# Optimization experiments

Hardware: AMD Instinct MI355X
Metric: run time of the kernel (lower is better)

The kernel has to match this reference:

```python
import jax, jax.numpy as jnp
import numpy as np

LN_EPS = 1e-5
WINDOWS = (5, 10, 20)


def _rolling_vol_mean(returns, w):
    # returns: [B, L]; rolling unbiased std (torch.std, ddof=1) over window w,
    # then mean over all window positions -> [B, 1]
    B = returns.shape[0]
    z = jnp.zeros((B, 1), returns.dtype)
    c1 = jnp.concatenate([z, jnp.cumsum(returns, axis=1)], axis=1)
    c2 = jnp.concatenate([z, jnp.cumsum(returns * returns, axis=1)], axis=1)
    s1 = c1[:, w:] - c1[:, :-w]          # window sums      [B, L-w+1]
    s2 = c2[:, w:] - c2[:, :-w]          # window sq sums   [B, L-w+1]
    var = (s2 - s1 * s1 / w) / (w - 1)
    std = jnp.sqrt(jnp.maximum(var, 0.0))
    return jnp.mean(std, axis=1, keepdims=True)


def _layernorm(x, g, b):
    mu = jnp.mean(x, axis=-1, keepdims=True)
    v = jnp.mean((x - mu) ** 2, axis=-1, keepdims=True)
    return (x - mu) / jnp.sqrt(v + LN_EPS) * g + b


def setup_inputs() -> dict:
    key = jax.random.key(0)
    ks = jax.random.split(key, 8)
    B, S, F = 4096, 4096, 1
    input_dim, hidden = 64, 256
    h2 = hidden // 2
    price_series = jax.random.uniform(ks[0], (B, S, F), jnp.float32) + 0.5
    sd = 0.02
    return {
        "price_series": price_series,
        "W1": jax.random.normal(ks[1], (input_dim, h2), jnp.float32) * sd,
        "b1": jnp.zeros((h2,), jnp.float32),
        "g1": jnp.ones((h2,), jnp.float32),
        "be1": jnp.zeros((h2,), jnp.float32),
        "W2": jax.random.normal(ks[2], (h2, h2), jnp.float32) * sd,
        "b2": jnp.zeros((h2,), jnp.float32),
        "g2": jnp.ones((h2,), jnp.float32),
        "be2": jnp.zeros((h2,), jnp.float32),
        "Wc1": jax.random.normal(ks[3], (hidden, 64), jnp.float32) * sd,
        "bc1": jnp.zeros((64,), jnp.float32),
        "Wc2": jax.random.normal(ks[4], (64, 4), jnp.float32) * sd,
        "bc2": jnp.zeros((4,), jnp.float32),
    }


def reference(price_series, W1, b1, g1, be1, W2, b2, g2, be2, Wc1, bc1, Wc2, bc2):
    input_dim = W1.shape[0]
    # features == 1 path: log returns
    safe_prices = jnp.clip(price_series, 1e-8, None)
    log_prices = jnp.log(safe_prices)
    returns = (log_prices[:, 1:, 0] - log_prices[:, :-1, 0])  # [B, S-1]

    vol_feats = [_rolling_vol_mean(returns, w) for w in WINDOWS]
    vol = jnp.concatenate(vol_feats, axis=1)                  # [B, 3]
    B = vol.shape[0]
    pad = jnp.zeros((B, input_dim - vol.shape[1]), vol.dtype)
    vol = jnp.concatenate([vol, pad], axis=1)                 # [B, input_dim]

    h = _layernorm(jax.nn.relu(vol @ W1 + b1), g1, be1)       # [B, h2]
    h2f = _layernorm(jax.nn.relu(h @ W2 + b2), g2, be2)       # [B, h2]
    combined = jnp.concatenate([h, h2f], axis=1)              # [B, hidden]
    logits = jax.nn.relu(combined @ Wc1 + bc1) @ Wc2 + bc2    # dropout = identity at eval
    regime = jax.nn.softmax(logits, axis=1)
    return combined, regime
```

## Files before the change

kernel.cpp:

```cpp
#include <hip/hip_runtime.h>
#include <math.h>

constexpr int S   = 4096;
constexpr int L   = S - 1;
constexpr int H2  = 128;
constexpr int HID = 256;
constexpr int NPOS = 16;
constexpr int WMAX = 20;
constexpr int RMAX = NPOS + WMAX - 1;
constexpr float LN_EPS = 1e-5f;

__device__ __forceinline__ float fast_sqrt(float x) { return __builtin_amdgcn_sqrtf(x); }
__device__ __forceinline__ float fast_rsqrt(float x) { return __builtin_amdgcn_rsqf(x); }

__device__ __forceinline__ float2 block_sum2(float a, float b, int tid, float* red8) {
    #pragma unroll
    for (int off = 32; off; off >>= 1) {
        a += __shfl_down(a, off);
        b += __shfl_down(b, off);
    }
    if ((tid & 63) == 0) { red8[(tid >> 6) * 2] = a; red8[(tid >> 6) * 2 + 1] = b; }
    __syncthreads();
    float2 r = make_float2(red8[0] + red8[2] + red8[4] + red8[6],
                           red8[1] + red8[3] + red8[5] + red8[7]);
    __syncthreads();
    return r;
}

template<int W>
__device__ __forceinline__ float window_acc(const float (&rr)[RMAX], int t0) {
    float s1 = 0.f, s2 = 0.f;
    #pragma unroll
    for (int j = 0; j < W; ++j) { s1 += rr[j]; s2 = fmaf(rr[j], rr[j], s2); }
    float acc = 0.f;
    constexpr float invw   = 1.f / (float)W;
    constexpr float invwm1 = 1.f / (float)(W - 1);
    const int n = L - W + 1;
    #pragma unroll
    for (int i = 0; i < NPOS; ++i) {
        if (t0 + i < n) {
            float var = (s2 - s1 * s1 * invw) * invwm1;
            acc += fast_sqrt(fmaxf(var, 0.f));
        }
        if (i < NPOS - 1) {
            float xin = rr[i + W], xout = rr[i];
            s1 += xin - xout;
            s2 += fmaf(xin, xin, -(xout * xout));
        }
    }
    return acc;
}

__global__ __launch_bounds__(256)
void vol_fused(const float* __restrict__ prices,
               const float* __restrict__ W1,  const float* __restrict__ b1,
               const float* __restrict__ g1,  const float* __restrict__ be1,
               const float* __restrict__ W2,  const float* __restrict__ b2,
               const float* __restrict__ g2,  const float* __restrict__ be2,
               const float* __restrict__ Wc1, const float* __restrict__ bc1,
               const float* __restrict__ Wc2, const float* __restrict__ bc2,
               float* __restrict__ out_combined, float* __restrict__ out_regime)
{
    __shared__ __align__(16) float lp[S + 40];
    __shared__ __align__(16) float part[1024];
    __shared__ float red8[8];
    __shared__ float redv[16];
    __shared__ float comb[HID];
    __shared__ float vols[4];

    const int tid = threadIdx.x;
    const int b   = blockIdx.x;

    const float4* prow = reinterpret_cast<const float4*>(prices + (size_t)b * S);
    #pragma unroll
    for (int i = 0; i < S / (4 * 256); ++i) {
        int idx = tid + i * 256;
        float4 v = prow[idx];
        lp[idx * 4 + 0] = __logf(fmaxf(v.x, 1e-8f));
        lp[idx * 4 + 1] = __logf(fmaxf(v.y, 1e-8f));
        lp[idx * 4 + 2] = __logf(fmaxf(v.z, 1e-8f));
        lp[idx * 4 + 3] = __logf(fmaxf(v.w, 1e-8f));
    }
    if (tid < 40) lp[S + tid] = 0.f;
    __syncthreads();

    const int t0 = tid * NPOS;
    float lpv[RMAX + 1];
    #pragma unroll
    for (int i = 0; i < (RMAX + 1) / 4; ++i) {
        float4 v = *reinterpret_cast<const float4*>(&lp[t0 + 4 * i]);
        lpv[4 * i + 0] = v.x; lpv[4 * i + 1] = v.y;
        lpv[4 * i + 2] = v.z; lpv[4 * i + 3] = v.w;
    }
    float rr[RMAX];
    #pragma unroll
    for (int i = 0; i < RMAX; ++i) rr[i] = lpv[i + 1] - lpv[i];

    float sum5  = window_acc<5>(rr, t0);
    float sum10 = window_acc<10>(rr, t0);
    float sum20 = window_acc<20>(rr, t0);

    #pragma unroll
    for (int off = 32; off; off >>= 1) {
        sum5  += __shfl_down(sum5,  off);
        sum10 += __shfl_down(sum10, off);
        sum20 += __shfl_down(sum20, off);
    }
    if ((tid & 63) == 0) {
        int w = tid >> 6;
        redv[w * 3 + 0] = sum5; redv[w * 3 + 1] = sum10; redv[w * 3 + 2] = sum20;
    }
    __syncthreads();
    if (tid < 3) {
        constexpr float sc[3] = { 1.f / (L - 5 + 1), 1.f / (L - 10 + 1), 1.f / (L - 20 + 1) };
        vols[tid] = (redv[tid] + redv[3 + tid] + redv[6 + tid] + redv[9 + tid]) * sc[tid];
    }
    __syncthreads();

    const float v0 = vols[0], v1 = vols[1], v2 = vols[2];

    float x = 0.f;
    if (tid < H2) {
        x = b1[tid];
        x = fmaf(v0, W1[0 * H2 + tid], x);
        x = fmaf(v1, W1[1 * H2 + tid], x);
        x = fmaf(v2, W1[2 * H2 + tid], x);
        x = fmaxf(x, 0.f);
    }
    float2 s = block_sum2((tid < H2) ? x : 0.f, (tid < H2) ? x * x : 0.f, tid, red8);
    {
        float mu  = s.x * (1.f / H2);
        float var = s.y * (1.f / H2) - mu * mu;
        if (tid < H2)
            comb[tid] = (x - mu) * fast_rsqrt(fmaxf(var, 0.f) + LN_EPS) * g1[tid] + be1[tid];
    }
    __syncthreads();

    {
        const int q = tid & 31, seg = tid >> 3 >> 2;
        const float* w2base = W2 + (size_t)(seg * 16) * H2 + q * 4;
        float ax = 0.f, ay = 0.f, az = 0.f, aw = 0.f;
        #pragma unroll
        for (int k = 0; k < 16; ++k) {
            float a = comb[seg * 16 + k];
            float4 w = *reinterpret_cast<const float4*>(w2base + (size_t)k * H2);
            ax = fmaf(a, w.x, ax); ay = fmaf(a, w.y, ay);
            az = fmaf(a, w.z, az); aw = fmaf(a, w.w, aw);
        }
        float4* p4 = reinterpret_cast<float4*>(part);
        p4[tid] = make_float4(ax, ay, az, aw);
    }
    __syncthreads();
    float x2 = 0.f;
    if (tid < H2) {
        float ssum = 0.f;
        #pragma unroll
        for (int sg = 0; sg < 8; ++sg) ssum += part[sg * 128 + tid];
        x2 = fmaxf(ssum + b2[tid], 0.f);
    }
    s = block_sum2((tid < H2) ? x2 : 0.f, (tid < H2) ? x2 * x2 : 0.f, tid, red8);
    {
        float mu  = s.x * (1.f / H2);
        float var = s.y * (1.f / H2) - mu * mu;
        if (tid < H2)
            comb[H2 + tid] = (x2 - mu) * fast_rsqrt(fmaxf(var, 0.f) + LN_EPS) * g2[tid] + be2[tid];
    }
    __syncthreads();

    out_combined[(size_t)b * HID + tid] = comb[tid];

    {
        const int q = tid & 15, seg = tid >> 4;
        const float* wcbase = Wc1 + (size_t)(seg * 16) * 64 + q * 4;
        float ax = 0.f, ay = 0.f, az = 0.f, aw = 0.f;
        #pragma unroll
        for (int k = 0; k < 16; ++k) {
            float a = comb[seg * 16 + k];
            float4 w = *reinterpret_cast<const float4*>(wcbase + (size_t)k * 64);
            ax = fmaf(a, w.x, ax); ay = fmaf(a, w.y, ay);
            az = fmaf(a, w.z, az); aw = fmaf(a, w.w, aw);
        }
        float4* p4 = reinterpret_cast<float4*>(part);
        p4[tid] = make_float4(ax, ay, az, aw);
    }
    __syncthreads();

    if (tid < 64) {
        float ssum = 0.f;
        #pragma unroll
        for (int sg = 0; sg < 16; ++sg) ssum += part[sg * 64 + tid];
        float c1 = fmaxf(ssum + bc1[tid], 0.f);

        float4 wrow = reinterpret_cast<const float4*>(Wc2)[tid];
        float lx = c1 * wrow.x, ly = c1 * wrow.y, lz = c1 * wrow.z, lw = c1 * wrow.w;
        #pragma unroll
        for (int off = 32; off; off >>= 1) {
            lx += __shfl_down(lx, off);
            ly += __shfl_down(ly, off);
            lz += __shfl_down(lz, off);
            lw += __shfl_down(lw, off);
        }
        if (tid == 0) {
            float4 bb = *reinterpret_cast<const float4*>(bc2);
            float l0 = lx + bb.x, l1 = ly + bb.y, l2 = lz + bb.z, l3 = lw + bb.w;
            float m  = fmaxf(fmaxf(l0, l1), fmaxf(l2, l3));
            float e0 = __expf(l0 - m), e1 = __expf(l1 - m);
            float e2 = __expf(l2 - m), e3 = __expf(l3 - m);
            float inv = 1.f / (e0 + e1 + e2 + e3);
            reinterpret_cast<float4*>(out_regime)[b] =
                make_float4(e0 * inv, e1 * inv, e2 * inv, e3 * inv);
        }
    }
}

extern "C" void kernel_launch(void* const* d_in, const int* in_sizes, int n_in,
                              void* d_out, int out_size, void* d_ws, size_t ws_size,
                              hipStream_t stream) {
    const float* prices = (const float*)d_in[0];
    const float* W1  = (const float*)d_in[1];
    const float* b1  = (const float*)d_in[2];
    const float* g1  = (const float*)d_in[3];
    const float* be1 = (const float*)d_in[4];
    const float* W2  = (const float*)d_in[5];
    const float* b2  = (const float*)d_in[6];
    const float* g2  = (const float*)d_in[7];
    const float* be2 = (const float*)d_in[8];
    const float* Wc1 = (const float*)d_in[9];
    const float* bc1 = (const float*)d_in[10];
    const float* Wc2 = (const float*)d_in[11];
    const float* bc2 = (const float*)d_in[12];

    const int B = in_sizes[0] / S;
    float* out_combined = (float*)d_out;
    float* out_regime   = (float*)d_out + (size_t)B * HID;

    vol_fused<<<B, 256, 0, stream>>>(prices, W1, b1, g1, be1, W2, b2, g2, be2,
                                     Wc1, bc1, Wc2, bc2, out_combined, out_regime);
}
```

Measured before the change: 43.86 us.

## Process two rows per block with register prefix sums, dropping shared log buffer

Each block now handles two batch rows. Each thread loads its own overlapping slice of prices straight from global memory into registers and takes logs there, so the shared log-price staging buffer and its barrier are gone. Rolling window std is computed from per-thread prefix sums instead of three sliding accumulators, and the MLP stages are restructured so all 256 threads work on both rows at once, amortizing weight loads. The cost is redundant global loads and log computations for the overlapping window halo, plus higher register pressure under the new occupancy hint.

```diff
diff --git a/kernel.cpp b/kernel.cpp
--- a/kernel.cpp
+++ b/kernel.cpp
@@ -1,198 +1,200 @@
 #include <hip/hip_runtime.h>
 #include <math.h>
 
-constexpr int S   = 4096;
-constexpr int L   = S - 1;
-constexpr int H2  = 128;
-constexpr int HID = 256;
+constexpr int S    = 4096;
+constexpr int L    = S - 1;
+constexpr int H2   = 128;
+constexpr int HID  = 256;
 constexpr int NPOS = 16;
-constexpr int WMAX = 20;
-constexpr int RMAX = NPOS + WMAX - 1;
+constexpr int ROWS = 2;
 constexpr float LN_EPS = 1e-5f;
 
-__device__ __forceinline__ float fast_sqrt(float x) { return __builtin_amdgcn_sqrtf(x); }
+constexpr int N5  = L - 5 + 1;
+constexpr int N10 = L - 10 + 1;
+constexpr int N20 = L - 20 + 1;
+
+__device__ __forceinline__ float fast_sqrt(float x)  { return __builtin_amdgcn_sqrtf(x); }
 __device__ __forceinline__ float fast_rsqrt(float x) { return __builtin_amdgcn_rsqf(x); }
 
-__device__ __forceinline__ float2 block_sum2(float a, float b, int tid, float* red8) {
-    #pragma unroll
-    for (int off = 32; off; off >>= 1) {
-        a += __shfl_down(a, off);
-        b += __shfl_down(b, off);
-    }
-    if ((tid & 63) == 0) { red8[(tid >> 6) * 2] = a; red8[(tid >> 6) * 2 + 1] = b; }
-    __syncthreads();
-    float2 r = make_float2(red8[0] + red8[2] + red8[4] + red8[6],
-                           red8[1] + red8[3] + red8[5] + red8[7]);
-    __syncthreads();
-    return r;
+template<int W>
+__device__ __forceinline__ float wstd(const float (&c1)[36], const float (&c2)[36], int i) {
+    constexpr float aw = 1.f / (float)(W - 1);
+    constexpr float bw = 1.f / ((float)W * (float)(W - 1));
+    float s1 = c1[i + W] - c1[i];
+    float s2 = c2[i + W] - c2[i];
+    float t  = fmaf(-(s1 * bw), s1, s2 * aw);
+    return fast_sqrt(fmaxf(t, 0.f));
 }
 
-template<int W>
-__device__ __forceinline__ float window_acc(const float (&rr)[RMAX], int t0) {
-    float s1 = 0.f, s2 = 0.f;
-    #pragma unroll
-    for (int j = 0; j < W; ++j) { s1 += rr[j]; s2 = fmaf(rr[j], rr[j], s2); }
-    float acc = 0.f;
-    constexpr float invw   = 1.f / (float)W;
-    constexpr float invwm1 = 1.f / (float)(W - 1);
-    const int n = L - W + 1;
-    #pragma unroll
-    for (int i = 0; i < NPOS; ++i) {
-        if (t0 + i < n) {
-            float var = (s2 - s1 * s1 * invw) * invwm1;
-            acc += fast_sqrt(fmaxf(var, 0.f));
-        }
-        if (i < NPOS - 1) {
-            float xin = rr[i + W], xout = rr[i];
-            s1 += xin - xout;
-            s2 += fmaf(xin, xin, -(xout * xout));
-        }
-    }
-    return acc;
-}
-
-__global__ __launch_bounds__(256)
-void vol_fused(const float* __restrict__ prices,
-               const float* __restrict__ W1,  const float* __restrict__ b1,
-               const float* __restrict__ g1,  const float* __restrict__ be1,
-               const float* __restrict__ W2,  const float* __restrict__ b2,
-               const float* __restrict__ g2,  const float* __restrict__ be2,
-               const float* __restrict__ Wc1, const float* __restrict__ bc1,
-               const float* __restrict__ Wc2, const float* __restrict__ bc2,
-               float* __restrict__ out_combined, float* __restrict__ out_regime)
+__global__ __launch_bounds__(256, 4)
+void vol_fused2(const float* __restrict__ prices,
+                const float* __restrict__ W1,  const float* __restrict__ b1,
+                const float* __restrict__ g1,  const float* __restrict__ be1,
+                const float* __restrict__ W2,  const float* __restrict__ b2,
+                const float* __restrict__ g2,  const float* __restrict__ be2,
+                const float* __restrict__ Wc1, const float* __restrict__ bc1,
+                const float* __restrict__ Wc2, const float* __restrict__ bc2,
+                float* __restrict__ out_combined, float* __restrict__ out_regime)
 {
-    __shared__ __align__(16) float lp[S + 40];
-    __shared__ __align__(16) float part[1024];
-    __shared__ float red8[8];
-    __shared__ float redv[16];
-    __shared__ float comb[HID];
-    __shared__ float vols[4];
+    __shared__ __align__(16) float fbuf[ROWS * HID];
+    __shared__ __align__(16) float partb[1024];
+    __shared__ float redw[ROWS][4][3];
+    __shared__ float vols_sh[ROWS][4];
+    __shared__ float c1s_unused[4];
 
     const int tid = threadIdx.x;
-    const int b   = blockIdx.x;
-
-    const float4* prow = reinterpret_cast<const float4*>(prices + (size_t)b * S);
-    #pragma unroll
-    for (int i = 0; i < S / (4 * 256); ++i) {
-        int idx = tid + i * 256;
-        float4 v = prow[idx];
-        lp[idx * 4 + 0] = __logf(fmaxf(v.x, 1e-8f));
-        lp[idx * 4 + 1] = __logf(fmaxf(v.y, 1e-8f));
-        lp[idx * 4 + 2] = __logf(fmaxf(v.z, 1e-8f));
-        lp[idx * 4 + 3] = __logf(fmaxf(v.w, 1e-8f));
-    }
-    if (tid < 40) lp[S + tid] = 0.f;
-    __syncthreads();
-
-    const int t0 = tid * NPOS;
-    float lpv[RMAX + 1];
-    #pragma unroll
-    for (int i = 0; i < (RMAX + 1) / 4; ++i) {
-        float4 v = *reinterpret_cast<const float4*>(&lp[t0 + 4 * i]);
-        lpv[4 * i + 0] = v.x; lpv[4 * i + 1] = v.y;
-        lpv[4 * i + 2] = v.z; lpv[4 * i + 3] = v.w;
-    }
-    float rr[RMAX];
-    #pragma unroll
-    for (int i = 0; i < RMAX; ++i) rr[i] = lpv[i + 1] - lpv[i];
-
-    float sum5  = window_acc<5>(rr, t0);
-    float sum10 = window_acc<10>(rr, t0);
-    float sum20 = window_acc<20>(rr, t0);
-
-    #pragma unroll
-    for (int off = 32; off; off >>= 1) {
-        sum5  += __shfl_down(sum5,  off);
-        sum10 += __shfl_down(sum10, off);
-        sum20 += __shfl_down(sum20, off);
-    }
-    if ((tid & 63) == 0) {
-        int w = tid >> 6;
-        redv[w * 3 + 0] = sum5; redv[w * 3 + 1] = sum10; redv[w * 3 + 2] = sum20;
-    }
-    __syncthreads();
-    if (tid < 3) {
-        constexpr float sc[3] = { 1.f / (L - 5 + 1), 1.f / (L - 10 + 1), 1.f / (L - 20 + 1) };
-        vols[tid] = (redv[tid] + redv[3 + tid] + redv[6 + tid] + redv[9 + tid]) * sc[tid];
-    }
-    __syncthreads();
-
-    const float v0 = vols[0], v1 = vols[1], v2 = vols[2];
-
-    float x = 0.f;
-    if (tid < H2) {
-        x = b1[tid];
-        x = fmaf(v0, W1[0 * H2 + tid], x);
-        x = fmaf(v1, W1[1 * H2 + tid], x);
-        x = fmaf(v2, W1[2 * H2 + tid], x);
-        x = fmaxf(x, 0.f);
-    }
-    float2 s = block_sum2((tid < H2) ? x : 0.f, (tid < H2) ? x * x : 0.f, tid, red8);
-    {
-        float mu  = s.x * (1.f / H2);
-        float var = s.y * (1.f / H2) - mu * mu;
-        if (tid < H2)
-            comb[tid] = (x - mu) * fast_rsqrt(fmaxf(var, 0.f) + LN_EPS) * g1[tid] + be1[tid];
-    }
-    __syncthreads();
-
-    {
-        const int q = tid & 31, seg = tid >> 3 >> 2;
-        const float* w2base = W2 + (size_t)(seg * 16) * H2 + q * 4;
+    const int w   = tid >> 6;
+    const int r0  = blockIdx.x * ROWS;
+
+    #pragma unroll 1
+    for (int r = 0; r < ROWS; ++r) {
+        const float4* p4 = reinterpret_cast<const float4*>(prices + (size_t)(r0 + r) * S);
+        float v[36];
+        #pragma unroll
+        for (int j = 0; j < 9; ++j) {
+            int sl = tid * 4 + j;
+            sl = sl < 1024 ? sl : 1023;
+            float4 f = p4[sl];
+            v[4 * j + 0] = f.x; v[4 * j + 1] = f.y;
+            v[4 * j + 2] = f.z; v[4 * j + 3] = f.w;
+        }
+        #pragma unroll
+        for (int i = 0; i < 36; ++i) v[i] = __logf(fmaxf(v[i], 1e-8f));
+
+        float c1[36], c2[36];
+        c1[0] = 0.f; c2[0] = 0.f;
+        #pragma unroll
+        for (int k = 1; k < 36; ++k) {
+            float d = v[k] - v[k - 1];
+            c1[k] = c1[k - 1] + d;
+            c2[k] = fmaf(d, d, c2[k - 1]);
+        }
+
+        const int t0 = tid * NPOS;
+        float sum5 = 0.f, sum10 = 0.f, sum20 = 0.f;
+        if (t0 + NPOS <= N20) {
+            #pragma unroll
+            for (int i = 0; i < NPOS; ++i) {
+                sum5  += wstd<5>(c1, c2, i);
+                sum10 += wstd<10>(c1, c2, i);
+                sum20 += wstd<20>(c1, c2, i);
+            }
+        } else {
+            #pragma unroll
+            for (int i = 0; i < NPOS; ++i) {
+                float s5 = wstd<5>(c1, c2, i), s10 = wstd<10>(c1, c2, i), s20 = wstd<20>(c1, c2, i);
+                if (t0 + i < N5)  sum5  += s5;
+                if (t0 + i < N10) sum10 += s10;
+                if (t0 + i < N20) sum20 += s20;
+            }
+        }
+        #pragma unroll
+        for (int off = 32; off; off >>= 1) {
+            sum5  += __shfl_down(sum5,  off);
+            sum10 += __shfl_down(sum10, off);
+            sum20 += __shfl_down(sum20, off);
+        }
+        if ((tid & 63) == 0) {
+            redw[r][w][0] = sum5; redw[r][w][1] = sum10; redw[r][w][2] = sum20;
+        }
+    }
+    __syncthreads();
+    if (tid < ROWS * 3) {
+        int r = tid / 3, k = tid % 3;
+        constexpr float sc[3] = { 1.f / N5, 1.f / N10, 1.f / N20 };
+        vols_sh[r][k] = (redw[r][0][k] + redw[r][1][k] + redw[r][2][k] + redw[r][3][k]) * sc[k];
+    }
+    __syncthreads();
+
+    const int c  = tid & 127;
+    const int rw = tid >> 7;
+    float x = fmaxf(fmaf(vols_sh[rw][2], W1[2 * H2 + c],
+                    fmaf(vols_sh[rw][1], W1[H2 + c],
+                    fmaf(vols_sh[rw][0], W1[c], b1[c]))), 0.f);
+    {
+        float s = x, sq = x * x;
+        #pragma unroll
+        for (int off = 32; off; off >>= 1) { s += __shfl_down(s, off); sq += __shfl_down(sq, off); }
+        if ((tid & 63) == 0) { redw[0][w][0] = s; redw[0][w][1] = sq; }
+    }
+    __syncthreads();
+    {
+        float ss = redw[0][rw * 2][0] + redw[0][rw * 2 + 1][0];
+        float sq = redw[0][rw * 2][1] + redw[0][rw * 2 + 1][1];
+        float mu = ss * (1.f / H2);
+        float var = sq * (1.f / H2) - mu * mu;
+        float rs = fast_rsqrt(fmaxf(var, 0.f) + LN_EPS);
+        fbuf[rw * HID + c] = (x - mu) * rs * g1[c] + be1[c];
+    }
+    __syncthreads();
+
+    {
+        const int q = tid & 31, r2 = (tid >> 5) & 1, kq = tid >> 6;
+        const float* wb = W2 + (size_t)(kq * 32) * H2 + q * 4;
+        const float* ab = &fbuf[r2 * HID + kq * 32];
         float ax = 0.f, ay = 0.f, az = 0.f, aw = 0.f;
-        #pragma unroll
-        for (int k = 0; k < 16; ++k) {
-            float a = comb[seg * 16 + k];
-            float4 w = *reinterpret_cast<const float4*>(w2base + (size_t)k * H2);
-            ax = fmaf(a, w.x, ax); ay = fmaf(a, w.y, ay);
-            az = fmaf(a, w.z, az); aw = fmaf(a, w.w, aw);
-        }
-        float4* p4 = reinterpret_cast<float4*>(part);
-        p4[tid] = make_float4(ax, ay, az, aw);
-    }
-    __syncthreads();
-    float x2 = 0.f;
-    if (tid < H2) {
-        float ssum = 0.f;
-        #pragma unroll
-        for (int sg = 0; sg < 8; ++sg) ssum += part[sg * 128 + tid];
-        x2 = fmaxf(ssum + b2[tid], 0.f);
-    }
-    s = block_sum2((tid < H2) ? x2 : 0.f, (tid < H2) ? x2 * x2 : 0.f, tid, red8);
-    {
-        float mu  = s.x * (1.f / H2);
-        float var = s.y * (1.f / H2) - mu * mu;
-        if (tid < H2)
-            comb[H2 + tid] = (x2 - mu) * fast_rsqrt(fmaxf(var, 0.f) + LN_EPS) * g2[tid] + be2[tid];
-    }
-    __syncthreads();
-
-    out_combined[(size_t)b * HID + tid] = comb[tid];
-
-    {
-        const int q = tid & 15, seg = tid >> 4;
-        const float* wcbase = Wc1 + (size_t)(seg * 16) * 64 + q * 4;
+        #pragma unroll 8
+        for (int k = 0; k < 32; ++k) {
+            float a = ab[k];
+            float4 ww = *reinterpret_cast<const float4*>(wb + (size_t)k * H2);
+            ax = fmaf(a, ww.x, ax); ay = fmaf(a, ww.y, ay);
+            az = fmaf(a, ww.z, az); aw = fmaf(a, ww.w, aw);
+        }
+        reinterpret_cast<float4*>(partb)[tid] = make_float4(ax, ay, az, aw);
+    }
+    __syncthreads();
+    float x2;
+    {
+        const int qq = c >> 2, ci = c & 3;
+        float ss = partb[(0 * 64 + rw * 32 + qq) * 4 + ci] +
+                   partb[(1 * 64 + rw * 32 + qq) * 4 + ci] +
+                   partb[(2 * 64 + rw * 32 + qq) * 4 + ci] +
+                   partb[(3 * 64 + rw * 32 + qq) * 4 + ci];
+        x2 = fmaxf(ss + b2[c], 0.f);
+    }
+    {
+        float s = x2, sq = x2 * x2;
+        #pragma unroll
+        for (int off = 32; off; off >>= 1) { s += __shfl_down(s, off); sq += __shfl_down(sq, off); }
+        if ((tid & 63) == 0) { redw[0][w][0] = s; redw[0][w][1] = sq; }
+    }
+    __syncthreads();
+    {
+        float ss = redw[0][rw * 2][0] + redw[0][rw * 2 + 1][0];
+        float sq = redw[0][rw * 2][1] + redw[0][rw * 2 + 1][1];
+        float mu = ss * (1.f / H2);
+        float var = sq * (1.f / H2) - mu * mu;
+        float rs = fast_rsqrt(fmaxf(var, 0.f) + LN_EPS);
+        fbuf[rw * HID + H2 + c] = (x2 - mu) * rs * g2[c] + be2[c];
+    }
+    __syncthreads();
+
+    {
+        const int cq = tid & 15, r2 = (tid >> 4) & 1, kq = tid >> 5;
+        const float* wb = Wc1 + (size_t)(kq * 32) * 64 + cq * 4;
+        const float* ab = &fbuf[r2 * HID + kq * 32];
         float ax = 0.f, ay = 0.f, az = 0.f, aw = 0.f;
-        #pragma unroll
-        for (int k = 0; k < 16; ++k) {
-            float a = comb[seg * 16 + k];
-            float4 w = *reinterpret_cast<const float4*>(wcbase + (size_t)k * 64);
-            ax = fmaf(a, w.x, ax); ay = fmaf(a, w.y, ay);
-            az = fmaf(a, w.z, az); aw = fmaf(a, w.w, aw);
-        }
-        float4* p4 = reinterpret_cast<float4*>(part);
-        p4[tid] = make_float4(ax, ay, az, aw);
-    }
-    __syncthreads();
-
-    if (tid < 64) {
-        float ssum = 0.f;
-        #pragma unroll
-        for (int sg = 0; sg < 16; ++sg) ssum += part[sg * 64 + tid];
-        float c1 = fmaxf(ssum + bc1[tid], 0.f);
-
-        float4 wrow = reinterpret_cast<const float4*>(Wc2)[tid];
-        float lx = c1 * wrow.x, ly = c1 * wrow.y, lz = c1 * wrow.z, lw = c1 * wrow.w;
+        #pragma unroll 8
+        for (int k = 0; k < 32; ++k) {
+            float a = ab[k];
+            float4 ww = *reinterpret_cast<const float4*>(wb + (size_t)k * 64);
+            ax = fmaf(a, ww.x, ax); ay = fmaf(a, ww.y, ay);
+            az = fmaf(a, ww.z, az); aw = fmaf(a, ww.w, aw);
+        }
+        reinterpret_cast<float4*>(partb)[tid] = make_float4(ax, ay, az, aw);
+    }
+    __syncthreads();
+
+    if (tid < 128) {
+        const int r = tid >> 6, cc = tid & 63;
+        const int cq = cc >> 2, ci = cc & 3;
+        float ss = 0.f;
+        #pragma unroll
+        for (int kq = 0; kq < 8; ++kq)
+            ss += partb[(kq * 32 + r * 16 + cq) * 4 + ci];
+        float c1v = fmaxf(ss + bc1[cc], 0.f);
+        float4 wrow = reinterpret_cast<const float4*>(Wc2)[cc];
+        float lx = c1v * wrow.x, ly = c1v * wrow.y, lz = c1v * wrow.z, lw = c1v * wrow.w;
         #pragma unroll
         for (int off = 32; off; off >>= 1) {
             lx += __shfl_down(lx, off);
@@ -200,16 +202,22 @@
             lz += __shfl_down(lz, off);
             lw += __shfl_down(lw, off);
         }
-        if (tid == 0) {
+        if (cc == 0) {
             float4 bb = *reinterpret_cast<const float4*>(bc2);
             float l0 = lx + bb.x, l1 = ly + bb.y, l2 = lz + bb.z, l3 = lw + bb.w;
             float m  = fmaxf(fmaxf(l0, l1), fmaxf(l2, l3));
             float e0 = __expf(l0 - m), e1 = __expf(l1 - m);
             float e2 = __expf(l2 - m), e3 = __expf(l3 - m);
             float inv = 1.f / (e0 + e1 + e2 + e3);
-            reinterpret_cast<float4*>(out_regime)[b] =
+            reinterpret_cast<float4*>(out_regime)[r0 + r] =
                 make_float4(e0 * inv, e1 * inv, e2 * inv, e3 * inv);
         }
+    }
+
+    if (tid < 128) {
+        const int r = tid >> 6, c4 = tid & 63;
+        float4 vv = *reinterpret_cast<const float4*>(&fbuf[r * HID + c4 * 4]);
+        reinterpret_cast<float4*>(out_combined)[(size_t)(r0 + r) * 64 + c4] = vv;
     }
 }
 
@@ -234,6 +242,6 @@
     float* out_combined = (float*)d_out;
     float* out_regime   = (float*)d_out + (size_t)B * HID;
 
-    vol_fused<<<B, 256, 0, stream>>>(prices, W1, b1, g1, be1, W2, b2, g2, be2,
-                                     Wc1, bc1, Wc2, bc2, out_combined, out_regime);
+    vol_fused2<<<B / ROWS, 256, 0, stream>>>(prices, W1, b1, g1, be1, W2, b2, g2, be2,
+                                             Wc1, bc1, Wc2, bc2, out_combined, out_regime);
 }
```

New measurement: 91.25 us. 2.08x slower.
